# Performance work log

Measured on AMD Instinct MI355X. Metric: run time of the kernel, lower is better.

The kernel has to match this reference:

```python
import jax, jax.numpy as jnp
import numpy as np

LEAK = 0.2

def lrelu(v):
    return jnp.maximum(v, LEAK * v)

def setup_inputs() -> dict:
    key = jax.random.key(0)
    ks = jax.random.split(key, 7)
    N, C, H = 1000000, 128, 3
    return {
        "x": jax.random.normal(ks[0], (N, C), dtype=jnp.float32),
        "w_mu": jax.random.normal(ks[1], (C, H), dtype=jnp.float32),
        "w_cov": jax.random.normal(ks[2], (C, C, H), dtype=jnp.float32),
        "w_mu_out": jax.random.normal(ks[3], (H, 1), dtype=jnp.float32),
        "w_cov_out": jax.random.normal(ks[4], (H, 1), dtype=jnp.float32),
        "b_mu": jax.random.normal(ks[5], (H,), dtype=jnp.float32),
        "b_cov": jax.random.normal(ks[6], (H,), dtype=jnp.float32),
    }

def reference(x, w_mu, w_cov, w_mu_out, w_cov_out, b_mu, b_cov):
    # x: [N, C]
    N = x.shape[0]
    mu = jnp.mean(x, axis=0)               # [C]
    xs = x - mu                            # [N, C]
    # mean of outer products == (xs^T @ xs) / N; avoids [N, C, C] intermediate
    cov = jnp.einsum('ne,nt->et', xs, xs) / N   # [C, C]
    mu_h = mu @ w_mu + b_mu                      # [H]
    cov_h = jnp.einsum('et,eth->h', cov, w_cov) + b_cov  # [H]
    mu_h = lrelu(mu_h)
    cov_h = lrelu(cov_h)
    return mu_h @ w_mu_out + cov_h @ w_cov_out   # [1]
```

## Files before the change

### kernel.cpp

```cpp
#include <hip/hip_runtime.h>

typedef __attribute__((ext_vector_type(4))) float f32x4;
typedef __attribute__((ext_vector_type(16))) float f32x16;
typedef __attribute__((ext_vector_type(8))) short bf16x8;

#define BK 64
#define SROW 72
#define GRID 512
#define NTHR 512

__device__ __forceinline__ unsigned pack_hi(unsigned ua, unsigned ub) {
    return (ua >> 16) | (ub & 0xffff0000u);
}

__global__ __launch_bounds__(NTHR, 4)
void mainK(const float* __restrict__ x, float* __restrict__ ws, int nchunks)
{
    __shared__ short ht[128][SROW];
    __shared__ short lt[128][SROW];

    float* wsGh  = ws;
    float* wsGhl = ws + 16384;
    float* wsS   = ws + 32768;

    const int tid  = threadIdx.x;
    const int lane = tid & 63;
    const int wave = tid >> 6;
    const int c0   = 4 * (tid >> 4);
    const int k0   = 2 * (tid & 15);

    const int frc = lane & 31;
    const int frg = lane >> 5;

    f32x16 acc[4];
    #pragma unroll
    for (int j = 0; j < 4; ++j)
        #pragma unroll
        for (int r = 0; r < 16; ++r) acc[j][r] = 0.0f;

    float csum[4] = {0.f, 0.f, 0.f, 0.f};

    const bool isGh = (wave < 4);
    const int e0 = 32 * (wave & 3);

    int chunk = blockIdx.x;
    f32x4 v0, v1, v2, v3;
    {
        const float* p = x + (size_t)chunk * (BK * 128) + c0;
        v0 = *(const f32x4*)(p + (size_t)(k0     ) * 128);
        v1 = *(const f32x4*)(p + (size_t)(k0 + 1 ) * 128);
        v2 = *(const f32x4*)(p + (size_t)(k0 + 32) * 128);
        v3 = *(const f32x4*)(p + (size_t)(k0 + 33) * 128);
    }

    while (true) {
        __syncthreads();
        #pragma unroll
        for (int i = 0; i < 4; ++i) {
            float a = v0[i], b = v1[i], c = v2[i], d = v3[i];
            csum[i] += (a + b) + (c + d);
            unsigned ua = __float_as_uint(a), ub = __float_as_uint(b);
            unsigned uc = __float_as_uint(c), ud = __float_as_uint(d);
            unsigned la = __float_as_uint(a - __uint_as_float(ua & 0xffff0000u));
            unsigned lb = __float_as_uint(b - __uint_as_float(ub & 0xffff0000u));
            unsigned lc = __float_as_uint(c - __uint_as_float(uc & 0xffff0000u));
            unsigned ld = __float_as_uint(d - __uint_as_float(ud & 0xffff0000u));
            *(unsigned*)&ht[c0 + i][k0     ] = pack_hi(ua, ub);
            *(unsigned*)&ht[c0 + i][k0 + 32] = pack_hi(uc, ud);
            *(unsigned*)&lt[c0 + i][k0     ] = pack_hi(la, lb);
            *(unsigned*)&lt[c0 + i][k0 + 32] = pack_hi(lc, ld);
        }
        __syncthreads();

        const int next = chunk + GRID;
        const bool hasNext = next < nchunks;
        if (hasNext) {
            const float* p = x + (size_t)next * (BK * 128) + c0;
            v0 = *(const f32x4*)(p + (size_t)(k0     ) * 128);
            v1 = *(const f32x4*)(p + (size_t)(k0 + 1 ) * 128);
            v2 = *(const f32x4*)(p + (size_t)(k0 + 32) * 128);
            v3 = *(const f32x4*)(p + (size_t)(k0 + 33) * 128);
        }

        #pragma unroll
        for (int ks = 0; ks < 4; ++ks) {
            const int kb = ks * 16 + 8 * frg;
            if (isGh) {
                bf16x8 f0 = *(const bf16x8*)&ht[ 0 + frc][kb];
                bf16x8 f1 = *(const bf16x8*)&ht[32 + frc][kb];
                bf16x8 f2 = *(const bf16x8*)&ht[64 + frc][kb];
                bf16x8 f3 = *(const bf16x8*)&ht[96 + frc][kb];
                bf16x8 fa = (e0 == 0) ? f0 : (e0 == 32) ? f1 : (e0 == 64) ? f2 : f3;
                acc[0] = __builtin_amdgcn_mfma_f32_32x32x16_bf16(fa, f0, acc[0], 0, 0, 0);
                acc[1] = __builtin_amdgcn_mfma_f32_32x32x16_bf16(fa, f1, acc[1], 0, 0, 0);
                acc[2] = __builtin_amdgcn_mfma_f32_32x32x16_bf16(fa, f2, acc[2], 0, 0, 0);
                acc[3] = __builtin_amdgcn_mfma_f32_32x32x16_bf16(fa, f3, acc[3], 0, 0, 0);
            } else {
                bf16x8 fa = *(const bf16x8*)&ht[e0 + frc][kb];
                bf16x8 f0 = *(const bf16x8*)&lt[ 0 + frc][kb];
                bf16x8 f1 = *(const bf16x8*)&lt[32 + frc][kb];
                bf16x8 f2 = *(const bf16x8*)&lt[64 + frc][kb];
                bf16x8 f3 = *(const bf16x8*)&lt[96 + frc][kb];
                acc[0] = __builtin_amdgcn_mfma_f32_32x32x16_bf16(fa, f0, acc[0], 0, 0, 0);
                acc[1] = __builtin_amdgcn_mfma_f32_32x32x16_bf16(fa, f1, acc[1], 0, 0, 0);
                acc[2] = __builtin_amdgcn_mfma_f32_32x32x16_bf16(fa, f2, acc[2], 0, 0, 0);
                acc[3] = __builtin_amdgcn_mfma_f32_32x32x16_bf16(fa, f3, acc[3], 0, 0, 0);
            }
        }

        if (!hasNext) break;
        chunk = next;
    }

    float* dst = isGh ? wsGh : wsGhl;
    #pragma unroll
    for (int j = 0; j < 4; ++j)
        #pragma unroll
        for (int r = 0; r < 16; ++r) {
            const int row = e0 + (r & 3) + 8 * (r >> 2) + 4 * frg;
            const int col = 32 * j + frc;
            atomicAdd(&dst[row * 128 + col], acc[j][r]);
        }

    #pragma unroll
    for (int i = 0; i < 4; ++i) {
        float s = csum[i];
        #pragma unroll
        for (int off = 1; off < 16; off <<= 1) s += __shfl_xor(s, off);
        if ((lane & 15) == 0) atomicAdd(&wsS[c0 + i], s);
    }
}

__global__ void zeroK(float* __restrict__ ws) {
    int i = blockIdx.x * 256 + threadIdx.x;
    if (i < 32896) ws[i] = 0.0f;
}

__global__ void finishK(const float* __restrict__ ws,
                        const float* __restrict__ w_mu, const float* __restrict__ w_cov,
                        const float* __restrict__ w_mu_out, const float* __restrict__ w_cov_out,
                        const float* __restrict__ b_mu, const float* __restrict__ b_cov,
                        float* __restrict__ out, float invN)
{
    const float* Gh  = ws;
    const float* Ghl = ws + 16384;
    const float* S   = ws + 32768;
    __shared__ float lmu[128];
    __shared__ float red[8][6];

    const int tid = threadIdx.x;
    if (tid < 128) lmu[tid] = S[tid] * invN;
    __syncthreads();

    float a0 = 0.f, a1 = 0.f, a2 = 0.f;
    for (int p = tid; p < 16384; p += NTHR) {
        const int e = p >> 7, t = p & 127;
        const float g = (Gh[p] + Ghl[p] + Ghl[t * 128 + e]) * invN - lmu[e] * lmu[t];
        a0 += g * w_cov[3 * p + 0];
        a1 += g * w_cov[3 * p + 1];
        a2 += g * w_cov[3 * p + 2];
    }
    float m0 = 0.f, m1 = 0.f, m2 = 0.f;
    if (tid < 128) {
        const float mv = lmu[tid];
        m0 = mv * w_mu[3 * tid + 0];
        m1 = mv * w_mu[3 * tid + 1];
        m2 = mv * w_mu[3 * tid + 2];
    }
    #pragma unroll
    for (int off = 32; off > 0; off >>= 1) {
        a0 += __shfl_down(a0, off); a1 += __shfl_down(a1, off); a2 += __shfl_down(a2, off);
        m0 += __shfl_down(m0, off); m1 += __shfl_down(m1, off); m2 += __shfl_down(m2, off);
    }
    const int lane = tid & 63, wave = tid >> 6;
    if (lane == 0) {
        red[wave][0] = a0; red[wave][1] = a1; red[wave][2] = a2;
        red[wave][3] = m0; red[wave][4] = m1; red[wave][5] = m2;
    }
    __syncthreads();
    if (tid == 0) {
        float A[6] = {0, 0, 0, 0, 0, 0};
        for (int w = 0; w < 8; ++w)
            for (int q = 0; q < 6; ++q) A[q] += red[w][q];
        float r = 0.f;
        for (int h = 0; h < 3; ++h) {
            float ch = A[h] + b_cov[h];
            float mh = A[3 + h] + b_mu[h];
            ch = fmaxf(ch, 0.2f * ch);
            mh = fmaxf(mh, 0.2f * mh);
            r += mh * w_mu_out[h] + ch * w_cov_out[h];
        }
        out[0] = r;
    }
}

extern "C" void kernel_launch(void* const* d_in, const int* in_sizes, int n_in,
                              void* d_out, int out_size, void* d_ws, size_t ws_size,
                              hipStream_t stream) {
    const float* x         = (const float*)d_in[0];
    const float* w_mu      = (const float*)d_in[1];
    const float* w_cov     = (const float*)d_in[2];
    const float* w_mu_out  = (const float*)d_in[3];
    const float* w_cov_out = (const float*)d_in[4];
    const float* b_mu      = (const float*)d_in[5];
    const float* b_cov     = (const float*)d_in[6];
    float* out = (float*)d_out;
    float* ws  = (float*)d_ws;

    const int N = in_sizes[0] / 128;
    const int nchunks = N / BK;

    zeroK<<<129, 256, 0, stream>>>(ws);
    mainK<<<GRID, NTHR, 0, stream>>>(x, ws, nchunks);
    finishK<<<1, NTHR, 0, stream>>>(ws, w_mu, w_cov, w_mu_out, w_cov_out,
                                    b_mu, b_cov, out, 1.0f / (float)N);
}
```

Before: 762.0 us.

## Fuse w_cov contraction into main kernel and drop zeroing kernel and atomics

Each block now contracts its partial Gram tiles with w_cov in registers and writes only three per-block partial sums plus per-block column sums, instead of atomically adding 32K floats into a global workspace. This removes the zeroing kernel launch and the heavy atomic traffic, and the finish kernel reduces the per-block partials and subtracts the mean-outer-product term. The global prefetch is also moved ahead of the second barrier. The cost is extra strided w_cov reads per block in the epilogue and a serial per-block reduction in the single-block finish kernel.

```diff
diff --git a/kernel.cpp b/kernel.cpp
--- a/kernel.cpp
+++ b/kernel.cpp
@@ -14,14 +14,12 @@
 }
 
 __global__ __launch_bounds__(NTHR, 4)
-void mainK(const float* __restrict__ x, float* __restrict__ ws, int nchunks)
+void mainK(const float* __restrict__ x, const float* __restrict__ w_cov,
+           float* __restrict__ ws, int nchunks)
 {
     __shared__ short ht[128][SROW];
     __shared__ short lt[128][SROW];
-
-    float* wsGh  = ws;
-    float* wsGhl = ws + 16384;
-    float* wsS   = ws + 32768;
+    __shared__ float red[8][4];
 
     const int tid  = threadIdx.x;
     const int lane = tid & 63;
@@ -70,7 +68,6 @@
             *(unsigned*)&lt[c0 + i][k0     ] = pack_hi(la, lb);
             *(unsigned*)&lt[c0 + i][k0 + 32] = pack_hi(lc, ld);
         }
-        __syncthreads();
 
         const int next = chunk + GRID;
         const bool hasNext = next < nchunks;
@@ -81,6 +78,7 @@
             v2 = *(const f32x4*)(p + (size_t)(k0 + 32) * 128);
             v3 = *(const f32x4*)(p + (size_t)(k0 + 33) * 128);
         }
+        __syncthreads();
 
         #pragma unroll
         for (int ks = 0; ks < 4; ++ks) {
@@ -112,54 +110,87 @@
         chunk = next;
     }
 
-    float* dst = isGh ? wsGh : wsGhl;
+    float wsum0 = 0.f, wsum1 = 0.f, wsum2 = 0.f;
     #pragma unroll
     for (int j = 0; j < 4; ++j)
         #pragma unroll
         for (int r = 0; r < 16; ++r) {
             const int row = e0 + (r & 3) + 8 * (r >> 2) + 4 * frg;
             const int col = 32 * j + frc;
-            atomicAdd(&dst[row * 128 + col], acc[j][r]);
-        }
+            const float g = acc[j][r];
+            const float* wp = w_cov + 3 * (row * 128 + col);
+            float w0 = wp[0], w1 = wp[1], w2 = wp[2];
+            if (!isGh) {
+                const float* wq = w_cov + 3 * (col * 128 + row);
+                w0 += wq[0]; w1 += wq[1]; w2 += wq[2];
+            }
+            wsum0 += g * w0; wsum1 += g * w1; wsum2 += g * w2;
+        }
+    #pragma unroll
+    for (int off = 32; off > 0; off >>= 1) {
+        wsum0 += __shfl_down(wsum0, off);
+        wsum1 += __shfl_down(wsum1, off);
+        wsum2 += __shfl_down(wsum2, off);
+    }
+    if (lane == 0) { red[wave][0] = wsum0; red[wave][1] = wsum1; red[wave][2] = wsum2; }
+    __syncthreads();
+    if (tid == 0) {
+        float s0 = 0.f, s1 = 0.f, s2 = 0.f;
+        for (int w = 0; w < 8; ++w) { s0 += red[w][0]; s1 += red[w][1]; s2 += red[w][2]; }
+        float* wc = ws + GRID * 128 + (size_t)blockIdx.x * 4;
+        wc[0] = s0; wc[1] = s1; wc[2] = s2;
+    }
 
     #pragma unroll
     for (int i = 0; i < 4; ++i) {
         float s = csum[i];
         #pragma unroll
         for (int off = 1; off < 16; off <<= 1) s += __shfl_xor(s, off);
-        if ((lane & 15) == 0) atomicAdd(&wsS[c0 + i], s);
-    }
-}
-
-__global__ void zeroK(float* __restrict__ ws) {
-    int i = blockIdx.x * 256 + threadIdx.x;
-    if (i < 32896) ws[i] = 0.0f;
-}
-
-__global__ void finishK(const float* __restrict__ ws,
-                        const float* __restrict__ w_mu, const float* __restrict__ w_cov,
-                        const float* __restrict__ w_mu_out, const float* __restrict__ w_cov_out,
-                        const float* __restrict__ b_mu, const float* __restrict__ b_cov,
-                        float* __restrict__ out, float invN)
+        csum[i] = s;
+    }
+    if ((lane & 15) == 0) {
+        f32x4 st = { csum[0], csum[1], csum[2], csum[3] };
+        *(f32x4*)(ws + (size_t)blockIdx.x * 128 + c0) = st;
+    }
+}
+
+__global__ __launch_bounds__(NTHR)
+void finishK(const float* __restrict__ ws,
+             const float* __restrict__ w_mu, const float* __restrict__ w_cov,
+             const float* __restrict__ w_mu_out, const float* __restrict__ w_cov_out,
+             const float* __restrict__ b_mu, const float* __restrict__ b_cov,
+             float* __restrict__ out, float invN)
 {
-    const float* Gh  = ws;
-    const float* Ghl = ws + 16384;
-    const float* S   = ws + 32768;
+    __shared__ float tmp[4][128];
     __shared__ float lmu[128];
-    __shared__ float red[8][6];
+    __shared__ float red[8][12];
 
     const int tid = threadIdx.x;
-    if (tid < 128) lmu[tid] = S[tid] * invN;
-    __syncthreads();
-
-    float a0 = 0.f, a1 = 0.f, a2 = 0.f;
+
+    {
+        const int c = tid & 127, q = tid >> 7;
+        float s = 0.f;
+        for (int b = q; b < GRID; b += 4) s += ws[b * 128 + c];
+        tmp[q][c] = s;
+    }
+    __syncthreads();
+    if (tid < 128)
+        lmu[tid] = (tmp[0][tid] + tmp[1][tid] + tmp[2][tid] + tmp[3][tid]) * invN;
+    __syncthreads();
+
+    const float* wc = ws + GRID * 128;
+    float c0s = wc[tid * 4 + 0];
+    float c1s = wc[tid * 4 + 1];
+    float c2s = wc[tid * 4 + 2];
+
+    float q0 = 0.f, q1 = 0.f, q2 = 0.f;
     for (int p = tid; p < 16384; p += NTHR) {
         const int e = p >> 7, t = p & 127;
-        const float g = (Gh[p] + Ghl[p] + Ghl[t * 128 + e]) * invN - lmu[e] * lmu[t];
-        a0 += g * w_cov[3 * p + 0];
-        a1 += g * w_cov[3 * p + 1];
-        a2 += g * w_cov[3 * p + 2];
-    }
+        const float m = lmu[e] * lmu[t];
+        const float* wp = w_cov + 3 * p;
+        q0 += m * wp[0]; q1 += m * wp[1]; q2 += m * wp[2];
+    }
+
     float m0 = 0.f, m1 = 0.f, m2 = 0.f;
     if (tid < 128) {
         const float mv = lmu[tid];
@@ -167,25 +198,28 @@
         m1 = mv * w_mu[3 * tid + 1];
         m2 = mv * w_mu[3 * tid + 2];
     }
+
     #pragma unroll
     for (int off = 32; off > 0; off >>= 1) {
-        a0 += __shfl_down(a0, off); a1 += __shfl_down(a1, off); a2 += __shfl_down(a2, off);
-        m0 += __shfl_down(m0, off); m1 += __shfl_down(m1, off); m2 += __shfl_down(m2, off);
+        c0s += __shfl_down(c0s, off); c1s += __shfl_down(c1s, off); c2s += __shfl_down(c2s, off);
+        q0  += __shfl_down(q0,  off); q1  += __shfl_down(q1,  off); q2  += __shfl_down(q2,  off);
+        m0  += __shfl_down(m0,  off); m1  += __shfl_down(m1,  off); m2  += __shfl_down(m2,  off);
     }
     const int lane = tid & 63, wave = tid >> 6;
     if (lane == 0) {
-        red[wave][0] = a0; red[wave][1] = a1; red[wave][2] = a2;
-        red[wave][3] = m0; red[wave][4] = m1; red[wave][5] = m2;
+        red[wave][0] = c0s; red[wave][1] = c1s; red[wave][2] = c2s;
+        red[wave][3] = q0;  red[wave][4] = q1;  red[wave][5] = q2;
+        red[wave][6] = m0;  red[wave][7] = m1;  red[wave][8] = m2;
     }
     __syncthreads();
     if (tid == 0) {
-        float A[6] = {0, 0, 0, 0, 0, 0};
+        float A[9] = {0,0,0,0,0,0,0,0,0};
         for (int w = 0; w < 8; ++w)
-            for (int q = 0; q < 6; ++q) A[q] += red[w][q];
+            for (int q = 0; q < 9; ++q) A[q] += red[w][q];
         float r = 0.f;
         for (int h = 0; h < 3; ++h) {
-            float ch = A[h] + b_cov[h];
-            float mh = A[3 + h] + b_mu[h];
+            float ch = A[h] * invN - A[3 + h] + b_cov[h];
+            float mh = A[6 + h] + b_mu[h];
             ch = fmaxf(ch, 0.2f * ch);
             mh = fmaxf(mh, 0.2f * mh);
             r += mh * w_mu_out[h] + ch * w_cov_out[h];
@@ -210,8 +244,7 @@
     const int N = in_sizes[0] / 128;
     const int nchunks = N / BK;
 
-    zeroK<<<129, 256, 0, stream>>>(ws);
-    mainK<<<GRID, NTHR, 0, stream>>>(x, ws, nchunks);
+    mainK<<<GRID, NTHR, 0, stream>>>(x, w_cov, ws, nchunks);
     finishK<<<1, NTHR, 0, stream>>>(ws, w_mu, w_cov, w_mu_out, w_cov_out,
                                     b_mu, b_cov, out, 1.0f / (float)N);
 }
```

Result: slower. 796.9 us (+4.6%).
